# Optimization experiments

Measured on AMD Instinct MI355X. Metric: run time of the kernel, lower is better.

Reference implementation:

```python
import jax, jax.numpy as jnp
import numpy as np

B, L, C, V = 16, 600, 256, 256
OUT_SEQ = 6000
KSZ = 5
DILATIONS = (1, 2, 4)
N_BLOCKS = 10
COND = 256  # speaker(128) + noise(128)
TEMP = 10.0
EPS = 1e-5


def _ccbn(x, cond, gw, gb, bw, bb):
    # x: (B, C, L); conditional batch-norm: per-channel stats over (batch, length),
    # gamma/beta predicted from condition vector.
    mu = jnp.mean(x, axis=(0, 2), keepdims=True)
    var = jnp.var(x, axis=(0, 2), keepdims=True)
    xn = (x - mu) * jax.lax.rsqrt(var + EPS)
    gamma = 1.0 + cond @ gw + gb  # (B, C)
    beta = cond @ bw + bb         # (B, C)
    return xn * gamma[:, :, None] + beta[:, :, None]


def _conv1d(x, w, b, dil=1):
    # x: (B, C_in, L); w: (C_out, C_in, K)
    y = jax.lax.conv_general_dilated(
        x, w, window_strides=(1,), padding='SAME', rhs_dilation=(dil,),
        dimension_numbers=('NCH', 'OIH', 'NCH'))
    return y + b[None, :, None]


def setup_inputs() -> dict:
    key = jax.random.key(0)
    ks = jax.random.split(key, 20)
    s = 0.02
    inp = {
        'inputs': jax.random.randint(ks[0], (B, L), 0, V),
        'speaker_embeddings': jax.random.normal(ks[1], (B, 128), jnp.float32),
        'noise': jax.random.normal(ks[2], (B, 128), jnp.float32),
        'emb': jax.random.normal(ks[3], (V, C), jnp.float32) * s,
        # 10 blocks x 3 dilated convs
        'conv_w': jax.random.normal(ks[4], (N_BLOCKS, 3, C, C, KSZ), jnp.float32) * s,
        'conv_b': jnp.zeros((N_BLOCKS, 3, C), jnp.float32),
        # CCBN projections per conv (gamma/beta from condition)
        'g_w': jax.random.normal(ks[5], (N_BLOCKS, 3, COND, C), jnp.float32) * s,
        'g_b': jnp.zeros((N_BLOCKS, 3, C), jnp.float32),
        'b_w': jax.random.normal(ks[6], (N_BLOCKS, 3, COND, C), jnp.float32) * s,
        'b_b': jnp.zeros((N_BLOCKS, 3, C), jnp.float32),
        # TokenLength head: 2 CCBNs + conv1 (256->256,k1) + conv2 (256->1,k1)
        'tl_g_w': jax.random.normal(ks[7], (2, COND, C), jnp.float32) * s,
        'tl_g_b': jnp.zeros((2, C), jnp.float32),
        'tl_b_w': jax.random.normal(ks[8], (2, COND, C), jnp.float32) * s,
        'tl_b_b': jnp.zeros((2, C), jnp.float32),
        'tl_conv1_w': jax.random.normal(ks[9], (C, C, 1), jnp.float32) * s,
        'tl_conv1_b': jnp.zeros((C,), jnp.float32),
        'tl_conv2_w': jax.random.normal(ks[10], (1, C, 1), jnp.float32) * s,
        'tl_conv2_b': jnp.zeros((1,), jnp.float32),
    }
    return inp


def reference(inputs, speaker_embeddings, noise, emb, conv_w, conv_b,
              g_w, g_b, b_w, b_b, tl_g_w, tl_g_b, tl_b_w, tl_b_b,
              tl_conv1_w, tl_conv1_b, tl_conv2_w, tl_conv2_b):
    cond = jnp.concatenate([speaker_embeddings, noise], axis=-1)  # (B, COND)
    x = emb[inputs]                    # (B, L, C)
    x = jnp.transpose(x, (0, 2, 1))    # (B, C, L)

    # 10 unaligned blocks: residual stacks of CCBN -> ReLU -> dilated conv
    for blk in range(N_BLOCKS):
        y = x
        for j, d in enumerate(DILATIONS):
            y = jax.nn.relu(_ccbn(y, cond, g_w[blk, j], g_b[blk, j], b_w[blk, j], b_b[blk, j]))
            y = _conv1d(y, conv_w[blk, j], conv_b[blk, j], dil=d)
        x = x + y
    unaligned = x  # (B, C, L)

    # TokenLength head
    t = jax.nn.relu(_ccbn(unaligned, cond, tl_g_w[0], tl_g_b[0], tl_b_w[0], tl_b_b[0]))
    t = _conv1d(t, tl_conv1_w, tl_conv1_b)
    t = jax.nn.relu(_ccbn(t, cond, tl_g_w[1], tl_g_b[1], tl_b_w[1], tl_b_b[1]))
    t = _conv1d(t, tl_conv2_w, tl_conv2_b)  # (B, 1, L)
    token_lengths = jax.nn.relu(t[:, 0, :])  # (B, L)

    token_ends = jnp.cumsum(token_lengths, axis=-1)        # (B, L)
    token_centers = token_ends - token_lengths / 2.0        # (B, L)
    aligned_lengths = token_ends

    out_pos = jnp.arange(OUT_SEQ, dtype=jnp.float32)         # (OUT,)
    diff = token_centers[:, None, :] - out_pos[None, :, None]  # (B, OUT, L)
    logits = -(diff * diff) / TEMP
    weights = jax.nn.softmax(logits, axis=-1)                # (B, OUT, L)

    feats = jnp.transpose(unaligned, (0, 2, 1))              # (B, L, C)
    aligned_features = jnp.einsum('bol,blc->boc', weights, feats)  # (B, OUT, C)
    return aligned_features, aligned_lengths
```

## Files before the change

kernel.cpp:

```cpp
#include <hip/hip_runtime.h>
#include <math.h>
#include <stdint.h>

#define EPSv 1e-5f

typedef short short8 __attribute__((ext_vector_type(8)));
typedef float floatx4 __attribute__((ext_vector_type(4)));

__device__ __forceinline__ unsigned short f2bf(float x) {
  unsigned u = __float_as_uint(x);
  unsigned r = (u + 0x7fffu + ((u >> 16) & 1u)) >> 16;
  return (unsigned short)r;
}

__device__ __forceinline__ void gld_lds16(const void* g, void* l) {
  __builtin_amdgcn_global_load_lds(
      (const __attribute__((address_space(1))) unsigned*)(uintptr_t)g,
      (__attribute__((address_space(3))) unsigned*)(uintptr_t)l,
      16, 0, 0);
}

__global__ __launch_bounds__(256) void k_gb_part(const float* __restrict__ spk,
                             const float* __restrict__ noise,
                             const float* __restrict__ g_w, const float* __restrict__ b_w,
                             const float* __restrict__ tl_g_w, const float* __restrict__ tl_b_w,
                             float* __restrict__ gpart, float* __restrict__ bpart) {
  __shared__ float condl[16][32];
  int i = blockIdx.x, ks = blockIdx.y;
  int t = threadIdx.x;
  for (int idx = t; idx < 512; idx += 256) {
    int b = idx >> 5, kk = idx & 31;
    int k = ks*32 + kk;
    condl[b][kk] = (k < 128) ? spk[b*128 + k] : noise[b*128 + k - 128];
  }
  __syncthreads();
  const float *gw, *bw;
  if (i < 30) { gw = g_w + (size_t)i*65536; bw = b_w + (size_t)i*65536; }
  else        { gw = tl_g_w + (size_t)(i-30)*65536; bw = tl_b_w + (size_t)(i-30)*65536; }
  int co = t;
  float g[16], bt[16];
  #pragma unroll
  for (int b = 0; b < 16; ++b) { g[b] = 0.f; bt[b] = 0.f; }
  for (int kk = 0; kk < 32; ++kk) {
    float gwv = gw[(size_t)(ks*32 + kk)*256 + co];
    float bwv = bw[(size_t)(ks*32 + kk)*256 + co];
    #pragma unroll
    for (int b = 0; b < 16; ++b) {
      float cv = condl[b][kk];
      g[b]  = fmaf(cv, gwv, g[b]);
      bt[b] = fmaf(cv, bwv, bt[b]);
    }
  }
  size_t base = ((size_t)(i*8 + ks)*16)*256 + co;
  #pragma unroll
  for (int b = 0; b < 16; ++b) {
    gpart[base + (size_t)b*256] = g[b];
    bpart[base + (size_t)b*256] = bt[b];
  }
}

__global__ void k_gb_red(const float* __restrict__ gpart, const float* __restrict__ bpart,
                         const float* __restrict__ g_b, const float* __restrict__ b_b,
                         const float* __restrict__ tl_g_b, const float* __restrict__ tl_b_b,
                         float* __restrict__ gammas, float* __restrict__ betas) {
  int idx = blockIdx.x*256 + threadIdx.x;
  int i = idx >> 12, rem = idx & 4095;
  int co = rem & 255;
  float gs = 0.f, bs = 0.f;
  #pragma unroll
  for (int ks = 0; ks < 8; ++ks) {
    size_t p = ((size_t)(i*8 + ks) << 12) + rem;
    gs += gpart[p];
    bs += bpart[p];
  }
  float gbias = (i < 30) ? g_b[i*256 + co] : tl_g_b[(i-30)*256 + co];
  float bbias = (i < 30) ? b_b[i*256 + co] : tl_b_b[(i-30)*256 + co];
  gammas[idx] = 1.0f + gs + gbias;
  betas [idx] = bs + bbias;
}

template<int TAPS>
__device__ __forceinline__ void wprep_body(const float* __restrict__ src,
                                           unsigned short* __restrict__ dst,
                                           int cotile, int chunk, int t) {
  int cow = t >> 2, ci8 = (t & 3) * 8;
  const float* s0 = src + ((size_t)(cotile*64 + cow)*256 + chunk*32 + ci8)*TAPS;
  float v[8*TAPS];
  #pragma unroll
  for (int i = 0; i < 8*TAPS; ++i) v[i] = s0[i];
  unsigned short* dblk = dst + (size_t)cotile*(8*TAPS*4096) + (size_t)chunk*(TAPS*4096);
  #pragma unroll
  for (int tap = 0; tap < TAPS; ++tap) {
    unsigned hi2[4], lo2[4];
    #pragma unroll
    for (int jj = 0; jj < 4; ++jj) {
      float a = v[(jj*2+0)*TAPS + tap], b = v[(jj*2+1)*TAPS + tap];
      unsigned short ha = f2bf(a), hb = f2bf(b);
      unsigned short la = f2bf(a - __uint_as_float((unsigned)ha << 16));
      unsigned short lb = f2bf(b - __uint_as_float((unsigned)hb << 16));
      hi2[jj] = (unsigned)ha | ((unsigned)hb << 16);
      lo2[jj] = (unsigned)la | ((unsigned)lb << 16);
    }
    uint4 H; H.x = hi2[0]; H.y = hi2[1]; H.z = hi2[2]; H.w = hi2[3];
    uint4 L; L.x = lo2[0]; L.y = lo2[1]; L.z = lo2[2]; L.w = lo2[3];
    *(uint4*)(dblk + (size_t)(tap*2)*2048 + cow*32 + ci8) = H;
    *(uint4*)(dblk + (size_t)(tap*2+1)*2048 + cow*32 + ci8) = L;
  }
}

__global__ __launch_bounds__(256) void k_wprep(const float* __restrict__ conv_w,
                                               const float* __restrict__ tl_c1_w,
                                               unsigned short* __restrict__ wp) {
  int cc = blockIdx.x;
  int cotile = blockIdx.y >> 3, chunk = blockIdx.y & 7;
  if (cc == 30) wprep_body<1>(tl_c1_w, wp + (size_t)30*655360, cotile, chunk, threadIdx.x);
  else          wprep_body<5>(conv_w + (size_t)cc*327680, wp + (size_t)cc*655360, cotile, chunk, threadIdx.x);
}

__global__ void k_embed2(const int* __restrict__ inp, const float* __restrict__ emb,
                         float* __restrict__ x, float* __restrict__ statp) {
  int bx = blockIdx.x;
  int c = threadIdx.x;
  int r0 = bx * 120;
  float s = 0.f, s2 = 0.f;
  for (int r = 0; r < 120; ++r) {
    int row = inp[r0 + r];
    float v = emb[(size_t)row*256 + c];
    x[(size_t)(r0 + r)*256 + c] = v;
    s += v; s2 = fmaf(v, v, s2);
  }
  statp[(size_t)bx*512 + c] = s;
  statp[(size_t)bx*512 + 256 + c] = s2;
}

__global__ __launch_bounds__(256) void k_norm(const float* __restrict__ z,
                      const float* __restrict__ statp,
                      const float* __restrict__ gam, const float* __restrict__ bet,
                      unsigned short* __restrict__ zn) {
  __shared__ float s_sc[32];
  __shared__ float s_sh[32];
  __shared__ float red[2][32][8];
  int b = blockIdx.x, chunk = blockIdx.y, sub = blockIdx.z;
  int t = threadIdx.x;
  {
    int ch = t >> 3, g = t & 7;
    int c = chunk*32 + ch;
    float s = 0.f, s2 = 0.f;
    for (int p = g; p < 80; p += 8) {
      s  += statp[(size_t)p*512 + c];
      s2 += statp[(size_t)p*512 + 256 + c];
    }
    red[0][ch][g] = s; red[1][ch][g] = s2;
  }
  __syncthreads();
  if (t < 32) {
    float s = 0.f, s2 = 0.f;
    #pragma unroll
    for (int g = 0; g < 8; ++g) { s += red[0][t][g]; s2 += red[1][t][g]; }
    int c = chunk*32 + t;
    float mu = s * (1.0f/9600.0f);
    float var = s2 * (1.0f/9600.0f) - mu*mu;
    float rs = rsqrtf(var + EPSv);
    float scale = rs * gam[b*256 + c];
    s_sc[t] = scale;
    s_sh[t] = fmaf(-mu, scale, bet[b*256 + c]);
  }
  __syncthreads();
  int srow = t >> 3, fq = t & 7;
  float4 sc4 = *(const float4*)&s_sc[fq*4];
  float4 sh4 = *(const float4*)&s_sh[fq*4];
  unsigned short* zh = zn + ((size_t)b*8 + chunk)*54400 + fq*4;
  unsigned short* zl = zh + 27200;
  const float* zb = z + (size_t)b*600*256 + chunk*32 + fq*4;
  int r0 = sub*68;
  #pragma unroll
  for (int i = 0; i < 3; ++i) {
    int rr = i*32 + srow;
    if (rr < 68) {
      int r = r0 + rr;
      int l = r - 8;
      uint2 vh; vh.x = 0u; vh.y = 0u;
      uint2 vl; vl.x = 0u; vl.y = 0u;
      if (l >= 0 && l < 600) {
        float4 zv = *(const float4*)&zb[(size_t)l*256];
        float v0 = fmaxf(fmaf(zv.x, sc4.x, sh4.x), 0.f);
        float v1 = fmaxf(fmaf(zv.y, sc4.y, sh4.y), 0.f);
        float v2 = fmaxf(fmaf(zv.z, sc4.z, sh4.z), 0.f);
        float v3 = fmaxf(fmaf(zv.w, sc4.w, sh4.w), 0.f);
        unsigned short h0 = f2bf(v0), h1 = f2bf(v1), h2 = f2bf(v2), h3 = f2bf(v3);
        unsigned short e0 = f2bf(v0 - __uint_as_float((unsigned)h0 << 16));
        unsigned short e1 = f2bf(v1 - __uint_as_float((unsigned)h1 << 16));
        unsigned short e2 = f2bf(v2 - __uint_as_float((unsigned)h2 << 16));
        unsigned short e3 = f2bf(v3 - __uint_as_float((unsigned)h3 << 16));
        vh.x = (unsigned)h0 | ((unsigned)h1 << 16);
        vh.y = (unsigned)h2 | ((unsigned)h3 << 16);
        vl.x = (unsigned)e0 | ((unsigned)e1 << 16);
        vl.y = (unsigned)e2 | ((unsigned)e3 << 16);
      }
      *(uint2*)&zh[(size_t)r*40] = vh;
      *(uint2*)&zl[(size_t)r*40] = vl;
    }
  }
}

template<int TAPS>
__global__ __launch_bounds__(256, 3) void k_convm(const unsigned short* __restrict__ zn,
                        float* __restrict__ out, float* __restrict__ statp,
                        const unsigned short* __restrict__ wpc,
                        const float* __restrict__ bias, int dil, int mode) {
  __shared__ __align__(16) unsigned short Zhi[2][6144];
  __shared__ __align__(16) unsigned short Zlo[2][6144];
  __shared__ float lsum[32];
  __shared__ float lsq[32];
  int t = threadIdx.x;
  int bx = blockIdx.x;
  int b  = bx / 5;
  int l0 = (bx % 5) * 128;
  int y = blockIdx.y;
  int co0 = y * 32;
  int cobase = (y & 1) * 32;
  int PAD = ((TAPS - 1)/2) * dil;
  int w = t >> 6, lane = t & 63;
  int lsub = (w & 1) * 64, cosub = (w >> 1) * 16;
  int quad = lane >> 4, nlan = lane & 15;
  if (t < 32) { lsum[t] = 0.f; lsq[t] = 0.f; }

  floatx4 acc[4];
  #pragma unroll
  for (int mt = 0; mt < 4; ++mt) acc[mt] = (floatx4){0.f,0.f,0.f,0.f};

  const unsigned short* zbase = zn + (size_t)b*435200 + (size_t)(l0 - PAD + 8)*40 + (size_t)lane*8;
  int ar[4];
  #pragma unroll
  for (int mt = 0; mt < 4; ++mt) ar[mt] = (lsub + mt*16 + nlan) * 40 + quad * 8;

  #define STAGEZ(ch, bf) do {                                             \
    const unsigned short* srcp = zbase + (size_t)(ch)*54400;              \
    for (int i = w; i < 24; i += 4) {                                     \
      int p = (i >= 12) ? 1 : 0;                                          \
      int k = i - p*12;                                                   \
      gld_lds16(srcp + p*27200 + k*512, (p ? Zlo[bf] : Zhi[bf]) + k*512); \
    }                                                                     \
  } while (0)

  STAGEZ(0, 0);
  __syncthreads();

  for (int chunk = 0; chunk < 8; ++chunk) {
    int cb = chunk & 1;
    if (chunk < 7) STAGEZ(chunk + 1, cb ^ 1);
    const unsigned short* pch = wpc + (size_t)((y >> 1)*8 + chunk) * (TAPS*4096);
    short8 bh[TAPS], bl[TAPS];
    int cw = (cobase + cosub + nlan)*32 + quad*8;
    #pragma unroll
    for (int tap = 0; tap < TAPS; ++tap) {
      bh[tap] = *(const short8*)(pch + (size_t)(tap*2)*2048 + cw);
      bl[tap] = *(const short8*)(pch + (size_t)(tap*2+1)*2048 + cw);
    }
    #pragma unroll
    for (int tap = 0; tap < TAPS; ++tap) {
      int sh = tap * dil * 40;
      #pragma unroll
      for (int mt = 0; mt < 4; ++mt) {
        short8 ah = *(const short8*)&Zhi[cb][ar[mt] + sh];
        short8 al = *(const short8*)&Zlo[cb][ar[mt] + sh];
        acc[mt] = __builtin_amdgcn_mfma_f32_16x16x32_bf16(ah, bh[tap], acc[mt], 0, 0, 0);
        acc[mt] = __builtin_amdgcn_mfma_f32_16x16x32_bf16(ah, bl[tap], acc[mt], 0, 0, 0);
        acc[mt] = __builtin_amdgcn_mfma_f32_16x16x32_bf16(al, bh[tap], acc[mt], 0, 0, 0);
      }
    }
    __syncthreads();
  }
  #undef STAGEZ

  float bsv = bias[co0 + cosub + nlan];
  float ssum = 0.f, ssq = 0.f;
  #pragma unroll
  for (int mt = 0; mt < 4; ++mt) {
    #pragma unroll
    for (int r = 0; r < 4; ++r) {
      int l = l0 + lsub + mt*16 + quad*4 + r;
      if (l < 600) {
        float v = acc[mt][r] + bsv;
        float* dst = &out[((size_t)(b*600 + l))*256 + co0 + cosub + nlan];
        if (mode) v += *dst;
        *dst = v;
        ssum += v;
        ssq = fmaf(v, v, ssq);
      }
    }
  }
  ssum += __shfl_xor(ssum, 16, 64);
  ssum += __shfl_xor(ssum, 32, 64);
  ssq  += __shfl_xor(ssq, 16, 64);
  ssq  += __shfl_xor(ssq, 32, 64);
  if (quad == 0) {
    atomicAdd(&lsum[cosub + nlan], ssum);
    atomicAdd(&lsq [cosub + nlan], ssq);
  }
  __syncthreads();
  if (t < 32) {
    statp[(size_t)bx*512 + co0 + t] = lsum[t];
    statp[(size_t)bx*512 + 256 + co0 + t] = lsq[t];
  }
}

__global__ void k_statred(const float* __restrict__ sp, float* __restrict__ dst) {
  int idx = blockIdx.x*256 + threadIdx.x;
  float s = 0.f;
  for (int p = 0; p < 80; ++p) s += sp[(size_t)p*512 + idx];
  dst[idx] = s;
}

__global__ void k_tl2(const float* __restrict__ z, const float* __restrict__ stat,
                      const float* __restrict__ gam, const float* __restrict__ bet,
                      const float* __restrict__ w2, const float* __restrict__ b2,
                      float* __restrict__ tl) {
  int t = threadIdx.x;
  int row = blockIdx.x * 4 + (t >> 6);
  int lane = t & 63;
  int b = row / 600;
  float4 s1 = *(const float4*)&stat[lane*4];
  float4 s2 = *(const float4*)&stat[256 + lane*4];
  float4 gm = *(const float4*)&gam[b*256 + lane*4];
  float4 bt = *(const float4*)&bet[b*256 + lane*4];
  float sc[4], sh[4];
  {
    float sv[4] = {s1.x, s1.y, s1.z, s1.w};
    float qv[4] = {s2.x, s2.y, s2.z, s2.w};
    float gv[4] = {gm.x, gm.y, gm.z, gm.w};
    float bv[4] = {bt.x, bt.y, bt.z, bt.w};
    #pragma unroll
    for (int i = 0; i < 4; ++i) {
      float mu = sv[i] * (1.0f/9600.0f);
      float var = qv[i] * (1.0f/9600.0f) - mu*mu;
      float rs = rsqrtf(var + EPSv);
      sc[i] = rs * gv[i];
      sh[i] = fmaf(-mu, sc[i], bv[i]);
    }
  }
  float4 zr = *(const float4*)&z[(size_t)row*256 + lane*4];
  float4 wr = *(const float4*)&w2[lane*4];
  float z0 = fmaxf(fmaf(zr.x, sc[0], sh[0]), 0.f);
  float z1 = fmaxf(fmaf(zr.y, sc[1], sh[1]), 0.f);
  float z2 = fmaxf(fmaf(zr.z, sc[2], sh[2]), 0.f);
  float z3 = fmaxf(fmaf(zr.w, sc[3], sh[3]), 0.f);
  float s = z0*wr.x + z1*wr.y + z2*wr.z + z3*wr.w;
  for (int m = 32; m >= 1; m >>= 1) s += __shfl_xor(s, m, 64);
  if (lane == 0) tl[row] = fmaxf(s + b2[0], 0.f);
}

__global__ void k_cumsum(const float* __restrict__ tl, float* __restrict__ centers,
                         float* __restrict__ out_len) {
  int b = blockIdx.x; int lane = threadIdx.x;
  float carry = 0.f;
  for (int ch = 0; ch < 10; ++ch) {
    int l = ch*64 + lane;
    float v = (l < 600) ? tl[b*600 + l] : 0.f;
    float s = v;
    #pragma unroll
    for (int off = 1; off < 64; off <<= 1) {
      float n = __shfl_up(s, off, 64);
      if (lane >= off) s += n;
    }
    float ends = carry + s;
    if (l < 600) {
      centers[b*600 + l] = ends - 0.5f*v;
      out_len[b*600 + l] = ends;
    }
    carry = __shfl(ends, 63, 64);
  }
}

__global__ void k_tobf16(const float* __restrict__ x, unsigned short* __restrict__ fbT) {
  __shared__ unsigned short T[64*66];
  int b = blockIdx.x, lt = blockIdx.y, ct = blockIdx.z;
  int t = threadIdx.x;
  int i4 = t >> 6;
  int j = t & 63;
  #pragma unroll
  for (int r = 0; r < 16; ++r) {
    int li = i4*16 + r;
    int l = lt*64 + li;
    float v = (l < 600) ? x[((size_t)(b*600 + l))*256 + ct*64 + j] : 0.f;
    T[j*66 + li] = f2bf(v);
  }
  __syncthreads();
  int row = t >> 2, seg = (t & 3) * 16;
  unsigned vv[8];
  #pragma unroll
  for (int k = 0; k < 8; ++k)
    vv[k] = *(const unsigned*)&T[row*66 + seg + k*2];
  size_t dsth = ((size_t)(b*256 + ct*64 + row))*640 + lt*64 + seg;
  unsigned* du = (unsigned*)fbT;
  uint4 a; a.x = vv[0]; a.y = vv[1]; a.z = vv[2]; a.w = vv[3];
  uint4 c4; c4.x = vv[4]; c4.y = vv[5]; c4.z = vv[6]; c4.w = vv[7];
  *(uint4*)(du + dsth/2) = a;
  *(uint4*)(du + dsth/2 + 4) = c4;
}

__global__ __launch_bounds__(256, 4) void k_align2(const unsigned short* __restrict__ fbT,
                        const float* __restrict__ centers, float* __restrict__ outp) {
  __shared__ float cen[600];
  __shared__ float mrow[64];
  __shared__ float isum[64];
  __shared__ unsigned actm_s;
  __shared__ unsigned short Wt[2][64*80];
  int b = blockIdx.x;
  int o0 = blockIdx.y * 64;
  int t = threadIdx.x;
  int wv = t >> 6, lane = t & 63;
  for (int i = t; i < 600; i += 256) cen[i] = centers[b*600 + i];
  __syncthreads();

  if (wv == 0) {
    float opos_l = (float)(o0 + lane);
    float dmin = 3.0e38f;
    float Dos[10];
    #pragma unroll
    for (int ch = 0; ch < 10; ++ch) {
      float clo = cen[ch*64];
      float chi = cen[(ch*64 + 63 < 599) ? ch*64 + 63 : 599];
      float Do = fmaxf(fmaxf(clo - opos_l, opos_l - chi), 0.f);
      Dos[ch] = Do;
      dmin = fminf(dmin, Do);
    }
    float mo_l = -dmin*dmin*0.1f;
    mrow[lane] = mo_l;
    unsigned am = 0;
    #pragma unroll
    for (int ch = 0; ch < 10; ++ch) {
      bool near = (fmaf(-Dos[ch]*Dos[ch], 0.1f, -mo_l) >= -80.f);
      if (__ballot(near) != 0ull) am |= (1u << ch);
    }
    if (lane == 0) actm_s = am;
  }
  __syncthreads();

  floatx4 acc[4][4];
  #pragma unroll
  for (int i = 0; i < 4; ++i)
    #pragma unroll
    for (int j = 0; j < 4; ++j)
      acc[i][j] = (floatx4){0.f, 0.f, 0.f, 0.f};
  int quad = lane >> 4;
  int nlan = lane & 15;
  int oi_w = t >> 2;
  int sbase = t & 3;
  float mo = mrow[oi_w];
  float opos_w = (float)(o0 + oi_w);
  float psum = 0.f;
  const unsigned short* srcb = fbT + ((size_t)b*256)*640;
  const unsigned short* fbl = srcb + (size_t)(wv*64 + nlan)*640 + quad*8;
  unsigned actm = actm_s;

  #define STAGE_WT(CH, BF) do {                                              \
    int lcs = (CH) * 64;                                                     \
    _Pragma("unroll")                                                        \
    for (int sidx = 0; sidx < 2; ++sidx) {                                   \
      int seg = sbase + sidx*4;                                              \
      unsigned pk[4];                                                        \
      _Pragma("unroll")                                                      \
      for (int jj = 0; jj < 8; jj += 2) {                                    \
        int li = lcs + seg*8 + jj;                                           \
        float e0 = 0.f, e1 = 0.f;                                            \
        if (li < 600)     { float d = cen[li] - opos_w;     e0 = __expf(fmaf(-d*d, 0.1f, -mo)); } \
        if (li + 1 < 600) { float d = cen[li + 1] - opos_w; e1 = __expf(fmaf(-d*d, 0.1f, -mo)); } \
        psum += e0 + e1;                                                     \
        pk[jj>>1] = (unsigned)f2bf(e0) | ((unsigned)f2bf(e1) << 16);         \
      }                                                                      \
      uint4 v; v.x = pk[0]; v.y = pk[1]; v.z = pk[2]; v.w = pk[3];           \
      *(uint4*)&Wt[BF][oi_w*80 + seg*8] = v;                                 \
    }                                                                        \
  } while (0)

  int ch = __ffs(actm) - 1;
  int buf = 0;
  STAGE_WT(ch, 0);
  __syncthreads();

  while (ch >= 0) {
    unsigned rem = actm & ~((2u << ch) - 1u);
    int nxt = rem ? (__ffs(rem) - 1) : -1;
    int lc0 = ch * 64;
    short8 bfr[2][4];
    #pragma unroll
    for (int ks = 0; ks < 2; ++ks)
      #pragma unroll
      for (int nt = 0; nt < 4; ++nt)
        bfr[ks][nt] = *(const short8*)(fbl + (size_t)nt*16*640 + lc0 + ks*32);
    if (nxt >= 0) STAGE_WT(nxt, buf ^ 1);
    #pragma unroll
    for (int ks = 0; ks < 2; ++ks) {
      int ko = ks*32 + quad*8;
      short8 af[4];
      #pragma unroll
      for (int mt = 0; mt < 4; ++mt)
        af[mt] = *(const short8*)&Wt[buf][(mt*16 + nlan)*80 + ko];
      #pragma unroll
      for (int mt = 0; mt < 4; ++mt)
        #pragma unroll
        for (int nt = 0; nt < 4; ++nt)
          acc[mt][nt] = __builtin_amdgcn_mfma_f32_16x16x32_bf16(af[mt], bfr[ks][nt], acc[mt][nt], 0, 0, 0);
    }
    __syncthreads();
    ch = nxt; buf ^= 1;
  }
  #undef STAGE_WT

  psum += __shfl_xor(psum, 1, 64);
  psum += __shfl_xor(psum, 2, 64);
  if ((t & 3) == 0) isum[oi_w] = 1.0f / psum;
  __syncthreads();

  #pragma unroll
  for (int mt = 0; mt < 4; ++mt) {
    #pragma unroll
    for (int r = 0; r < 4; ++r) {
      int oi = mt*16 + quad*4 + r;
      int o = o0 + oi;
      if (o < 6000) {
        float sc = isum[oi];
        #pragma unroll
        for (int nt = 0; nt < 4; ++nt) {
          int c = wv*64 + nt*16 + nlan;
          outp[((size_t)b*6000 + o)*256 + c] = acc[mt][nt][r] * sc;
        }
      }
    }
  }
}

extern "C" void kernel_launch(void* const* d_in, const int* in_sizes, int n_in,
                              void* d_out, int out_size, void* d_ws, size_t ws_size,
                              hipStream_t stream) {
  const int*   inputs = (const int*)  d_in[0];
  const float* spk    = (const float*)d_in[1];
  const float* noise  = (const float*)d_in[2];
  const float* emb    = (const float*)d_in[3];
  const float* conv_w = (const float*)d_in[4];
  const float* conv_b = (const float*)d_in[5];
  const float* g_w    = (const float*)d_in[6];
  const float* g_b    = (const float*)d_in[7];
  const float* b_w    = (const float*)d_in[8];
  const float* b_b    = (const float*)d_in[9];
  const float* tl_g_w = (const float*)d_in[10];
  const float* tl_g_b = (const float*)d_in[11];
  const float* tl_b_w = (const float*)d_in[12];
  const float* tl_b_b = (const float*)d_in[13];
  const float* tl_c1_w = (const float*)d_in[14];
  const float* tl_c1_b = (const float*)d_in[15];
  const float* tl_c2_w = (const float*)d_in[16];
  const float* tl_c2_b = (const float*)d_in[17];
  float* out = (float*)d_out;

  float* ws = (float*)d_ws;
  float* x       = ws;
  float* A       = x + 2457600;
  float* Bf      = A + 2457600;
  float* gammas  = Bf + 2457600;
  float* betas   = gammas + 131072;
  float* statp   = betas + 131072;
  float* stat31  = statp + 81920;
  float* tl      = stat31 + 512;
  float* cen     = tl + 9600;
  unsigned short* wp = (unsigned short*)(cen + 9600);
  unsigned short* Zn = wp + (size_t)31*655360;
  unsigned short* fbT = (unsigned short*)Bf;
  float* gpart = (float*)Zn;
  float* bpart = gpart + 1048576;

  k_wprep<<<dim3(31, 32), dim3(256), 0, stream>>>(conv_w, tl_c1_w, wp);
  k_gb_part<<<dim3(32, 8), dim3(256), 0, stream>>>(spk, noise, g_w, b_w,
      tl_g_w, tl_b_w, gpart, bpart);
  k_gb_red<<<dim3(512), dim3(256), 0, stream>>>(gpart, bpart, g_b, b_b,
      tl_g_b, tl_b_b, gammas, betas);
  k_embed2<<<dim3(80), dim3(256), 0, stream>>>(inputs, emb, x, statp);

  const int dils[3] = {1, 2, 4};
  for (int blk = 0; blk < 10; ++blk) {
    const float* srcs[3] = {x, A, Bf};
    float*       dsts[3] = {A, Bf, x};
    for (int j = 0; j < 3; ++j) {
      int idx = blk*3 + j;
      int mode = (j == 2) ? 1 : 0;
      k_norm<<<dim3(16, 8, 10), dim3(256), 0, stream>>>(srcs[j],
          statp, gammas + idx*4096, betas + idx*4096, Zn);
      k_convm<5><<<dim3(80, 8), dim3(256), 0, stream>>>(Zn, dsts[j],
          statp, wp + (size_t)idx*655360, conv_b + idx*256, dils[j], mode);
    }
  }
  k_norm<<<dim3(16, 8, 10), dim3(256), 0, stream>>>(x,
      statp, gammas + 30*4096, betas + 30*4096, Zn);
  k_convm<1><<<dim3(80, 8), dim3(256), 0, stream>>>(Zn, A,
      statp, wp + (size_t)30*655360, tl_c1_b, 1, 0);
  k_statred<<<dim3(2), dim3(256), 0, stream>>>(statp, stat31);
  k_tl2<<<dim3(2400), dim3(256), 0, stream>>>(A, stat31,
      gammas + 31*4096, betas + 31*4096, tl_c2_w, tl_c2_b, tl);
  k_cumsum<<<dim3(16), dim3(64), 0, stream>>>(tl, cen, out + 24576000);
  k_tobf16<<<dim3(16, 10, 4), dim3(256), 0, stream>>>(x, fbT);
  k_align2<<<dim3(16, 94), dim3(256), 0, stream>>>(fbT, cen, out);
}
```

Measured before the change: 1.505 ms.

## Retile conv kernel to 64x64 output tiles with per-tap weight prefetch

Result: slower. 1.870 ms (+24.2%).

```diff
diff --git a/kernel.cpp b/kernel.cpp
--- a/kernel.cpp
+++ b/kernel.cpp
@@ -121,9 +121,9 @@
                          float* __restrict__ x, float* __restrict__ statp) {
   int bx = blockIdx.x;
   int c = threadIdx.x;
-  int r0 = bx * 120;
+  int r0 = bx * 60;
   float s = 0.f, s2 = 0.f;
-  for (int r = 0; r < 120; ++r) {
+  for (int r = 0; r < 60; ++r) {
     int row = inp[r0 + r];
     float v = emb[(size_t)row*256 + c];
     x[(size_t)(r0 + r)*256 + c] = v;
@@ -146,7 +146,7 @@
     int ch = t >> 3, g = t & 7;
     int c = chunk*32 + ch;
     float s = 0.f, s2 = 0.f;
-    for (int p = g; p < 80; p += 8) {
+    for (int p = g; p < 160; p += 8) {
       s  += statp[(size_t)p*512 + c];
       s2 += statp[(size_t)p*512 + 256 + c];
     }
@@ -204,41 +204,46 @@
 }
 
 template<int TAPS>
-__global__ __launch_bounds__(256, 3) void k_convm(const unsigned short* __restrict__ zn,
+__global__ __launch_bounds__(256, 4) void k_convm(const unsigned short* __restrict__ zn,
                         float* __restrict__ out, float* __restrict__ statp,
                         const unsigned short* __restrict__ wpc,
                         const float* __restrict__ bias, int dil, int mode) {
-  __shared__ __align__(16) unsigned short Zhi[2][6144];
-  __shared__ __align__(16) unsigned short Zlo[2][6144];
-  __shared__ float lsum[32];
-  __shared__ float lsq[32];
+  __shared__ __align__(16) unsigned short Zhi[2][3584];
+  __shared__ __align__(16) unsigned short Zlo[2][3584];
+  __shared__ float lsum[64];
+  __shared__ float lsq[64];
   int t = threadIdx.x;
   int bx = blockIdx.x;
-  int b  = bx / 5;
-  int l0 = (bx % 5) * 128;
+  int b  = bx / 10;
+  int l0 = (bx % 10) * 64;
   int y = blockIdx.y;
-  int co0 = y * 32;
-  int cobase = (y & 1) * 32;
+  int co0 = y * 64;
   int PAD = ((TAPS - 1)/2) * dil;
   int w = t >> 6, lane = t & 63;
-  int lsub = (w & 1) * 64, cosub = (w >> 1) * 16;
+  int lw = (w & 1) * 32, cw = (w >> 1) * 32;
   int quad = lane >> 4, nlan = lane & 15;
-  if (t < 32) { lsum[t] = 0.f; lsq[t] = 0.f; }
-
-  floatx4 acc[4];
-  #pragma unroll
-  for (int mt = 0; mt < 4; ++mt) acc[mt] = (floatx4){0.f,0.f,0.f,0.f};
+  if (t < 64) { lsum[t] = 0.f; lsq[t] = 0.f; }
+
+  floatx4 acc[2][2];
+  #pragma unroll
+  for (int mt = 0; mt < 2; ++mt)
+    #pragma unroll
+    for (int nt = 0; nt < 2; ++nt)
+      acc[mt][nt] = (floatx4){0.f,0.f,0.f,0.f};
 
   const unsigned short* zbase = zn + (size_t)b*435200 + (size_t)(l0 - PAD + 8)*40 + (size_t)lane*8;
-  int ar[4];
-  #pragma unroll
-  for (int mt = 0; mt < 4; ++mt) ar[mt] = (lsub + mt*16 + nlan) * 40 + quad * 8;
+  int ar[2];
+  #pragma unroll
+  for (int mt = 0; mt < 2; ++mt) ar[mt] = (lw + mt*16 + nlan) * 40 + quad * 8;
+  int cwo[2];
+  #pragma unroll
+  for (int nt = 0; nt < 2; ++nt) cwo[nt] = (cw + nt*16 + nlan)*32 + quad*8;
 
   #define STAGEZ(ch, bf) do {                                             \
     const unsigned short* srcp = zbase + (size_t)(ch)*54400;              \
-    for (int i = w; i < 24; i += 4) {                                     \
-      int p = (i >= 12) ? 1 : 0;                                          \
-      int k = i - p*12;                                                   \
+    for (int i = w; i < 14; i += 4) {                                     \
+      int p = (i >= 7) ? 1 : 0;                                           \
+      int k = i - p*7;                                                    \
       gld_lds16(srcp + p*27200 + k*512, (p ? Zlo[bf] : Zhi[bf]) + k*512); \
     }                                                                     \
   } while (0)
@@ -249,57 +254,78 @@
   for (int chunk = 0; chunk < 8; ++chunk) {
     int cb = chunk & 1;
     if (chunk < 7) STAGEZ(chunk + 1, cb ^ 1);
-    const unsigned short* pch = wpc + (size_t)((y >> 1)*8 + chunk) * (TAPS*4096);
-    short8 bh[TAPS], bl[TAPS];
-    int cw = (cobase + cosub + nlan)*32 + quad*8;
+    const unsigned short* pch = wpc + (size_t)(y*8 + chunk) * (TAPS*4096);
+    short8 bh[2][2], bl[2][2];
+    #pragma unroll
+    for (int nt = 0; nt < 2; ++nt) {
+      bh[0][nt] = *(const short8*)(pch + cwo[nt]);
+      bl[0][nt] = *(const short8*)(pch + 2048 + cwo[nt]);
+    }
     #pragma unroll
     for (int tap = 0; tap < TAPS; ++tap) {
-      bh[tap] = *(const short8*)(pch + (size_t)(tap*2)*2048 + cw);
-      bl[tap] = *(const short8*)(pch + (size_t)(tap*2+1)*2048 + cw);
-    }
-    #pragma unroll
-    for (int tap = 0; tap < TAPS; ++tap) {
+      int cur = tap & 1, nxt = cur ^ 1;
+      if (tap + 1 < TAPS) {
+        #pragma unroll
+        for (int nt = 0; nt < 2; ++nt) {
+          bh[nxt][nt] = *(const short8*)(pch + (size_t)((tap+1)*2)*2048 + cwo[nt]);
+          bl[nxt][nt] = *(const short8*)(pch + (size_t)((tap+1)*2+1)*2048 + cwo[nt]);
+        }
+      }
       int sh = tap * dil * 40;
       #pragma unroll
-      for (int mt = 0; mt < 4; ++mt) {
+      for (int mt = 0; mt < 2; ++mt) {
         short8 ah = *(const short8*)&Zhi[cb][ar[mt] + sh];
         short8 al = *(const short8*)&Zlo[cb][ar[mt] + sh];
-        acc[mt] = __builtin_amdgcn_mfma_f32_16x16x32_bf16(ah, bh[tap], acc[mt], 0, 0, 0);
-        acc[mt] = __builtin_amdgcn_mfma_f32_16x16x32_bf16(ah, bl[tap], acc[mt], 0, 0, 0);
-        acc[mt] = __builtin_amdgcn_mfma_f32_16x16x32_bf16(al, bh[tap], acc[mt], 0, 0, 0);
+        #pragma unroll
+        for (int nt = 0; nt < 2; ++nt) {
+          acc[mt][nt] = __builtin_amdgcn_mfma_f32_16x16x32_bf16(ah, bh[cur][nt], acc[mt][nt], 0, 0, 0);
+          acc[mt][nt] = __builtin_amdgcn_mfma_f32_16x16x32_bf16(ah, bl[cur][nt], acc[mt][nt], 0, 0, 0);
+          acc[mt][nt] = __builtin_amdgcn_mfma_f32_16x16x32_bf16(al, bh[cur][nt], acc[mt][nt], 0, 0, 0);
+        }
       }
     }
     __syncthreads();
   }
   #undef STAGEZ
 
-  float bsv = bias[co0 + cosub + nlan];
-  float ssum = 0.f, ssq = 0.f;
-  #pragma unroll
-  for (int mt = 0; mt < 4; ++mt) {
+  float bsv[2];
+  #pragma unroll
+  for (int nt = 0; nt < 2; ++nt) bsv[nt] = bias[co0 + cw + nt*16 + nlan];
+  float ssum[2] = {0.f, 0.f}, ssq[2] = {0.f, 0.f};
+  #pragma unroll
+  for (int mt = 0; mt < 2; ++mt) {
     #pragma unroll
     for (int r = 0; r < 4; ++r) {
-      int l = l0 + lsub + mt*16 + quad*4 + r;
+      int l = l0 + lw + mt*16 + quad*4 + r;
       if (l < 600) {
-        float v = acc[mt][r] + bsv;
-        float* dst = &out[((size_t)(b*600 + l))*256 + co0 + cosub + nlan];
-        if (mode) v += *dst;
-        *dst = v;
-        ssum += v;
-        ssq = fmaf(v, v, ssq);
+        #pragma unroll
+        for (int nt = 0; nt < 2; ++nt) {
+          float v = acc[mt][nt][r] + bsv[nt];
+          float* dst = &out[((size_t)(b*600 + l))*256 + co0 + cw + nt*16 + nlan];
+          if (mode) v += *dst;
+          *dst = v;
+          ssum[nt] += v;
+          ssq[nt] = fmaf(v, v, ssq[nt]);
+        }
       }
     }
   }
-  ssum += __shfl_xor(ssum, 16, 64);
-  ssum += __shfl_xor(ssum, 32, 64);
-  ssq  += __shfl_xor(ssq, 16, 64);
-  ssq  += __shfl_xor(ssq, 32, 64);
+  #pragma unroll
+  for (int nt = 0; nt < 2; ++nt) {
+    ssum[nt] += __shfl_xor(ssum[nt], 16, 64);
+    ssum[nt] += __shfl_xor(ssum[nt], 32, 64);
+    ssq[nt]  += __shfl_xor(ssq[nt], 16, 64);
+    ssq[nt]  += __shfl_xor(ssq[nt], 32, 64);
+  }
   if (quad == 0) {
-    atomicAdd(&lsum[cosub + nlan], ssum);
-    atomicAdd(&lsq [cosub + nlan], ssq);
-  }
-  __syncthreads();
-  if (t < 32) {
+    #pragma unroll
+    for (int nt = 0; nt < 2; ++nt) {
+      atomicAdd(&lsum[cw + nt*16 + nlan], ssum[nt]);
+      atomicAdd(&lsq [cw + nt*16 + nlan], ssq[nt]);
+    }
+  }
+  __syncthreads();
+  if (t < 64) {
     statp[(size_t)bx*512 + co0 + t] = lsum[t];
     statp[(size_t)bx*512 + 256 + co0 + t] = lsq[t];
   }
@@ -308,7 +334,7 @@
 __global__ void k_statred(const float* __restrict__ sp, float* __restrict__ dst) {
   int idx = blockIdx.x*256 + threadIdx.x;
   float s = 0.f;
-  for (int p = 0; p < 80; ++p) s += sp[(size_t)p*512 + idx];
+  for (int p = 0; p < 160; ++p) s += sp[(size_t)p*512 + idx];
   dst[idx] = s;
 }
 
@@ -575,7 +601,7 @@
       tl_g_w, tl_b_w, gpart, bpart);
   k_gb_red<<<dim3(512), dim3(256), 0, stream>>>(gpart, bpart, g_b, b_b,
       tl_g_b, tl_b_b, gammas, betas);
-  k_embed2<<<dim3(80), dim3(256), 0, stream>>>(inputs, emb, x, statp);
+  k_embed2<<<dim3(160), dim3(256), 0, stream>>>(inputs, emb, x, statp);
 
   const int dils[3] = {1, 2, 4};
   for (int blk = 0; blk < 10; ++blk) {
@@ -586,13 +612,13 @@
       int mode = (j == 2) ? 1 : 0;
       k_norm<<<dim3(16, 8, 10), dim3(256), 0, stream>>>(srcs[j],
           statp, gammas + idx*4096, betas + idx*4096, Zn);
-      k_convm<5><<<dim3(80, 8), dim3(256), 0, stream>>>(Zn, dsts[j],
+      k_convm<5><<<dim3(160, 4), dim3(256), 0, stream>>>(Zn, dsts[j],
           statp, wp + (size_t)idx*655360, conv_b + idx*256, dils[j], mode);
     }
   }
   k_norm<<<dim3(16, 8, 10), dim3(256), 0, stream>>>(x,
       statp, gammas + 30*4096, betas + 30*4096, Zn);
-  k_convm<1><<<dim3(80, 8), dim3(256), 0, stream>>>(Zn, A,
+  k_convm<1><<<dim3(160, 4), dim3(256), 0, stream>>>(Zn, A,
       statp, wp + (size_t)30*655360, tl_c1_b, 1, 0);
   k_statred<<<dim3(2), dim3(256), 0, stream>>>(statp, stat31);
   k_tl2<<<dim3(2400), dim3(256), 0, stream>>>(A, stat31,
```
